# Performance work log

Measured on AMD Instinct MI355X. Metric: run time of the kernel, lower is better.

The kernel has to match this reference:

```python
import jax, jax.numpy as jnp
import numpy as np

EPS = 1e-5
KH = KW = 3  # deformable kernel
K = KH * KW


def _offset_conv(w, woff, boff):
    # standard 3x3 conv, stride 1, padding 1, NCHW
    out = jax.lax.conv_general_dilated(
        w, woff, window_strides=(1, 1), padding='SAME',
        dimension_numbers=('NCHW', 'OIHW', 'NCHW'))
    return out + boff[None, :, None, None]


def _deform_conv(feat, offset, wd, bd):
    # feat: [B,C,H,W]; offset: [B,2K,H,W] with (dy,dx) pairs per kernel point
    B, C, H, W = feat.shape
    off = offset.reshape(B, K, 2, H, W)
    ii = jnp.arange(H, dtype=feat.dtype)[:, None]  # [H,1]
    jj = jnp.arange(W, dtype=feat.dtype)[None, :]  # [1,W]
    kk = jnp.arange(K)
    ky = (kk // KW - 1).astype(feat.dtype)[None, :, None, None]  # [1,K,1,1]
    kx = (kk % KW - 1).astype(feat.dtype)[None, :, None, None]
    py = ii[None, None] + ky + off[:, :, 0]  # [B,K,H,W] sample rows
    px = jj[None, None] + kx + off[:, :, 1]  # [B,K,H,W] sample cols

    featf = feat.reshape(B, C, H * W)
    y0 = jnp.floor(py)
    x0 = jnp.floor(px)
    sampled = jnp.zeros((B, C, K, H, W), dtype=feat.dtype)
    for dy in (0, 1):
        for dx in (0, 1):
            yc = y0 + dy
            xc = x0 + dx
            wgt = (1.0 - jnp.abs(py - yc)) * (1.0 - jnp.abs(px - xc))
            valid = (yc >= 0) & (yc <= H - 1) & (xc >= 0) & (xc <= W - 1)
            wgt = jnp.where(valid, wgt, 0.0)  # zero padding outside
            yi = jnp.clip(yc, 0, H - 1).astype(jnp.int32)
            xi = jnp.clip(xc, 0, W - 1).astype(jnp.int32)
            idx = (yi * W + xi).reshape(B, 1, K * H * W)
            vals = jnp.take_along_axis(featf, idx, axis=2).reshape(B, C, K, H, W)
            sampled = sampled + vals * wgt[:, None]
    # weighted 3x3 conv over sampled points
    out = jnp.einsum('bckhw,ock->bohw', sampled, wd.reshape(wd.shape[0], C, K))
    return out + bd[None, :, None, None]


def setup_inputs() -> dict:
    key = jax.random.key(0)
    ks = jax.random.split(key, 13)
    B, Cin, H, W = 8, 256, 96, 96
    Cm = 64
    s1 = 1.0 / np.sqrt(Cin)
    s3 = 1.0 / np.sqrt(Cm * 9)
    return {
        'x': jax.random.normal(ks[0], (B, Cin, H, W), jnp.float32),
        'w1': jax.random.normal(ks[1], (Cm, Cin), jnp.float32) * s1,
        'b1': jax.random.normal(ks[2], (Cm,), jnp.float32) * s1,
        'woff': jax.random.normal(ks[3], (18, Cm, 3, 3), jnp.float32) * s3,
        'boff': jax.random.normal(ks[4], (18,), jnp.float32) * s3,
        'wd': jax.random.normal(ks[5], (Cm, Cm, 3, 3), jnp.float32) * s3,
        'bd': jax.random.normal(ks[6], (Cm,), jnp.float32) * s3,
        'gamma': jnp.ones((Cm,), jnp.float32),
        'beta': jnp.zeros((Cm,), jnp.float32),
        'rmean': jnp.zeros((Cm,), jnp.float32),
        'rvar': jax.random.uniform(ks[7], (Cm,), jnp.float32, 0.5, 1.5),
        'w2': jax.random.normal(ks[8], (Cin, Cm), jnp.float32) / np.sqrt(Cm),
        'b2': jax.random.normal(ks[9], (Cin,), jnp.float32) / np.sqrt(Cm),
    }


def reference(x, w1, b1, woff, boff, wd, bd, gamma, beta, rmean, rvar, w2, b2):
    # pwconv1 (1x1)
    w = jnp.einsum('bchw,oc->bohw', x, w1) + b1[None, :, None, None]
    # deformable 3x3 conv with predicted offsets
    off = _offset_conv(w, woff, boff)
    w = _deform_conv(w, off, wd, bd)
    # BatchNorm (eval mode, running stats)
    inv = gamma / jnp.sqrt(rvar + EPS)
    w = w * inv[None, :, None, None] + (beta - rmean * inv)[None, :, None, None]
    # pwconv2 (1x1) + sigmoid gate
    w = jnp.einsum('bchw,oc->bohw', w, w2) + b2[None, :, None, None]
    return x * jax.nn.sigmoid(w)
```

## Files before the change

### kernel.cpp

```cpp
#include <hip/hip_runtime.h>
#include <math.h>

#define H 96
#define W 96
#define HW 9216
#define B 8
#define CIN 256
#define CM 64
#define NPOS (B*HW)
#define NBLK (NPOS/64)

__device__ __forceinline__ int xswiz(int n) { return (n & 7) * 144 + (n >> 3); }

typedef float  f32x4  __attribute__((ext_vector_type(4)));
typedef short  bf16x8 __attribute__((ext_vector_type(8)));

#define OFF_WDBO  0
#define OFF_BNS   9216
#define OFF_BNB   9280
#define OFF_WDB1  9344
#define OFF_WDB3  17536
#define OFF_WDB2  35968
#define OFF_FCL   44160
#define OFF_OFFS  4762752
#define OFF_VCL   6089856

__device__ __forceinline__ unsigned bfbits(float f) {
  union { float f; unsigned u; } c;
  c.f = f;
  return (c.u + 0x7FFFu + ((c.u >> 16) & 1u)) >> 16;
}
__device__ __forceinline__ short f2bf(float f) { return (short)bfbits(f); }
__device__ __forceinline__ unsigned pack2(float lo, float hi) {
  return bfbits(lo) | (bfbits(hi) << 16);
}

__global__ __launch_bounds__(256) void k0_prep(
    const float* __restrict__ w1, const float* __restrict__ woff,
    const float* __restrict__ wd, const float* __restrict__ w2,
    const float* __restrict__ gamma, const float* __restrict__ beta,
    const float* __restrict__ rmean, const float* __restrict__ rvar,
    float* __restrict__ ws) {
  int i = blockIdx.x * 256 + threadIdx.x;
  if (i < 18432) {
    int j = i;
    int j8 = j & 7, lane = (j >> 3) & 63, nt = (j >> 9) & 1, kc = j >> 10;
    int n = nt * 16 + (lane & 15);
    int c = (kc & 1) * 32 + ((lane >> 4) & 3) * 8 + j8;
    int ks = kc >> 1;
    ((short*)(ws + OFF_WDBO))[j] = (n < 18) ? f2bf(woff[(n * 64 + c) * 9 + ks]) : (short)0;
  } else if (i < 18496) {
    int o = i - 18432;
    float inv = gamma[o] / sqrtf(rvar[o] + 1e-5f);
    ws[OFF_BNS + o] = inv;
    ws[OFF_BNB + o] = beta[o] - rmean[o] * inv;
  } else if (i < 34880) {
    int j = i - 18496;
    int j8 = j & 7, lane = (j >> 3) & 63, nt = (j >> 9) & 3, kc = j >> 11;
    int n = nt * 16 + (lane & 15);
    int c = kc * 32 + ((lane >> 4) & 3) * 8 + j8;
    ((short*)(ws + OFF_WDB1))[j] = f2bf(w1[n * 256 + c]);
  } else if (i < 71744) {
    int j = i - 34880;
    int j8 = j & 7, lane = (j >> 3) & 63, nt = (j >> 9) & 3, kc = j >> 11;
    int n = nt * 16 + (lane & 15);
    int c = (kc & 1) * 32 + ((lane >> 4) & 3) * 8 + j8;
    int ks = kc >> 1;
    ((short*)(ws + OFF_WDB3))[j] = f2bf(wd[(n * 64 + c) * 9 + ks]);
  } else if (i < 88128) {
    int j = i - 71744;
    int j8 = j & 7, lane = (j >> 3) & 63, nt = (j >> 9) & 15, kc = j >> 13;
    int n = nt * 16 + (lane & 15);
    int c = kc * 32 + ((lane >> 4) & 3) * 8 + j8;
    ((short*)(ws + OFF_WDB2))[j] = f2bf(w2[n * 64 + c]);
  }
}

__global__ __launch_bounds__(256) void k1_pw1(
    const float* __restrict__ x, const short* __restrict__ wdb1,
    const float* __restrict__ b1, float* __restrict__ fcl) {
  __shared__ float sA[64 * 66];
  int t = threadIdx.x;
  int lane = t & 63;
  int qq = __builtin_amdgcn_readfirstlane(t >> 6);
  int quad = lane >> 4, l15 = lane & 15;
  int gpos0 = xswiz(blockIdx.x) * 64;
  int b = gpos0 / HW, hw0 = gpos0 - b * HW;
  const float* xp = x + (size_t)b * CIN * HW + (size_t)(quad * 8) * HW + hw0 + qq * 16 + l15;

  float v[8][8];
#pragma unroll
  for (int kc = 0; kc < 8; kc++)
#pragma unroll
    for (int jj = 0; jj < 8; jj++)
      v[kc][jj] = xp[(size_t)(kc * 32 + jj) * HW];

  f32x4 acc[4];
#pragma unroll
  for (int nt = 0; nt < 4; nt++) acc[nt] = (f32x4){0.f, 0.f, 0.f, 0.f};
#pragma unroll
  for (int kc = 0; kc < 8; kc++) {
    union { unsigned u[4]; bf16x8 f; } af;
    af.u[0] = pack2(v[kc][0], v[kc][1]); af.u[1] = pack2(v[kc][2], v[kc][3]);
    af.u[2] = pack2(v[kc][4], v[kc][5]); af.u[3] = pack2(v[kc][6], v[kc][7]);
#pragma unroll
    for (int nt = 0; nt < 4; nt++) {
      bf16x8 bf = ((const bf16x8*)wdb1)[(kc * 4 + nt) * 64 + lane];
      acc[nt] = __builtin_amdgcn_mfma_f32_16x16x32_bf16(af.f, bf, acc[nt], 0, 0, 0);
    }
  }
#pragma unroll
  for (int nt = 0; nt < 4; nt++) {
    int o = nt * 16 + l15;
#pragma unroll
    for (int reg = 0; reg < 4; reg++) {
      int m = qq * 16 + quad * 4 + reg;
      sA[m * 66 + o] = acc[nt][reg] + b1[o];
    }
  }
  __syncthreads();
  for (int rr = t; rr < 4096; rr += 256) {
    int p2 = rr >> 6, o2 = rr & 63;
    fcl[(size_t)(gpos0 + p2) * 64 + o2] = sA[p2 * 66 + o2];
  }
}

__global__ __launch_bounds__(256) void k2_off(
    const float* __restrict__ fcl, const short* __restrict__ wdbo,
    const float* __restrict__ boff, float* __restrict__ offs) {
  __shared__ float sP[64 * 34];
  int t = threadIdx.x;
  int lane = t & 63;
  int qq = __builtin_amdgcn_readfirstlane(t >> 6);
  int quad = lane >> 4, l15 = lane & 15;
  int gpos0 = xswiz(blockIdx.x) * 64;
  int b = gpos0 / HW, hw0 = gpos0 - b * HW;
  int m = qq * 16 + l15;
  int hw = hw0 + m, i = hw / W, j = hw - i * W;
  const float* base = fcl + (size_t)(gpos0 + m) * 64 + quad * 8;

  f32x4 acc[2];
  acc[0] = (f32x4){0.f, 0.f, 0.f, 0.f};
  acc[1] = (f32x4){0.f, 0.f, 0.f, 0.f};

  f32x4 va0, vb0, va1, vb1;
  bool okc;
  {
    okc = (i >= 1) && (j >= 1);
    const float* s = base + (okc ? (-W - 1) * 64 : 0);
    va0 = *(const f32x4*)(s);      vb0 = *(const f32x4*)(s + 4);
    va1 = *(const f32x4*)(s + 32); vb1 = *(const f32x4*)(s + 36);
  }
#pragma unroll
  for (int ks = 0; ks < 9; ks++) {
    f32x4 z = (f32x4){0.f, 0.f, 0.f, 0.f};
    f32x4 a0 = okc ? va0 : z, c0 = okc ? vb0 : z;
    f32x4 a1 = okc ? va1 : z, c1 = okc ? vb1 : z;
    union { unsigned u[4]; bf16x8 f; } f0, f1;
    f0.u[0] = pack2(a0[0], a0[1]); f0.u[1] = pack2(a0[2], a0[3]);
    f0.u[2] = pack2(c0[0], c0[1]); f0.u[3] = pack2(c0[2], c0[3]);
    f1.u[0] = pack2(a1[0], a1[1]); f1.u[1] = pack2(a1[2], a1[3]);
    f1.u[2] = pack2(c1[0], c1[1]); f1.u[3] = pack2(c1[2], c1[3]);
    if (ks < 8) {
      int kn = ks + 1, dy = kn / 3 - 1, dx = kn % 3 - 1;
      okc = ((unsigned)(i + dy) < (unsigned)H) && ((unsigned)(j + dx) < (unsigned)W);
      const float* s = base + (okc ? (dy * W + dx) * 64 : 0);
      va0 = *(const f32x4*)(s);      vb0 = *(const f32x4*)(s + 4);
      va1 = *(const f32x4*)(s + 32); vb1 = *(const f32x4*)(s + 36);
    }
    bf16x8 bf00 = ((const bf16x8*)wdbo)[((ks * 2 + 0) * 2 + 0) * 64 + lane];
    bf16x8 bf01 = ((const bf16x8*)wdbo)[((ks * 2 + 0) * 2 + 1) * 64 + lane];
    bf16x8 bf10 = ((const bf16x8*)wdbo)[((ks * 2 + 1) * 2 + 0) * 64 + lane];
    bf16x8 bf11 = ((const bf16x8*)wdbo)[((ks * 2 + 1) * 2 + 1) * 64 + lane];
    acc[0] = __builtin_amdgcn_mfma_f32_16x16x32_bf16(f0.f, bf00, acc[0], 0, 0, 0);
    acc[1] = __builtin_amdgcn_mfma_f32_16x16x32_bf16(f0.f, bf01, acc[1], 0, 0, 0);
    acc[0] = __builtin_amdgcn_mfma_f32_16x16x32_bf16(f1.f, bf10, acc[0], 0, 0, 0);
    acc[1] = __builtin_amdgcn_mfma_f32_16x16x32_bf16(f1.f, bf11, acc[1], 0, 0, 0);
  }
#pragma unroll
  for (int nt = 0; nt < 2; nt++)
#pragma unroll
    for (int reg = 0; reg < 4; reg++) {
      int mm = qq * 16 + quad * 4 + reg;
      sP[mm * 34 + nt * 16 + l15] = acc[nt][reg];
    }
  __syncthreads();
  for (int rr = t; rr < 18 * 64; rr += 256) {
    int o = rr >> 6, p = rr & 63;
    offs[((size_t)b * 18 + o) * HW + hw0 + p] = sP[p * 34 + o] + boff[o];
  }
}

__global__ __launch_bounds__(256, 3) void k3_deform(
    const float* __restrict__ fcl, const float* __restrict__ offs,
    const short* __restrict__ wdb3, const float* __restrict__ bd,
    const float* __restrict__ bns, const float* __restrict__ bnb,
    short* __restrict__ vclb) {
  __shared__ __align__(16) short sAb[2][64 * 72];
  __shared__ __align__(16) int2 tiw[576][4];
  int t = threadIdx.x;
  int lane = t & 63;
  int qq = __builtin_amdgcn_readfirstlane(t >> 6);
  int quad = lane >> 4, l15 = lane & 15;
  int mrow = qq * 16 + l15;
  int gpos0 = xswiz(blockIdx.x) * 64;
  int b = gpos0 / HW, hw0 = gpos0 - b * HW;
  int hw = hw0 + lane;
  int i = hw / W, j = hw - i * W;
  const float* ob = offs + (size_t)b * 18 * HW + hw;

  for (int k = qq; k < 9; k += 4) {
    float dy = ob[(2 * k + 0) * HW];
    float dx = ob[(2 * k + 1) * HW];
    float py = (float)(i + k / 3 - 1) + dy;
    float px = (float)(j + k % 3 - 1) + dx;
    float y0f = floorf(py), x0f = floorf(px);
    int y0 = (int)y0f, x0 = (int)x0f;
    float fy = py - y0f, fx = px - x0f;
    float w00 = (1.f - fy) * (1.f - fx), w01 = (1.f - fy) * fx;
    float w10 = fy * (1.f - fx), w11 = fy * fx;
    bool vy0 = (y0 >= 0) && (y0 < H), vy1 = (y0 + 1 >= 0) && (y0 + 1 < H);
    bool vx0 = (x0 >= 0) && (x0 < W), vx1 = (x0 + 1 >= 0) && (x0 + 1 < W);
    if (!(vy0 && vx0)) w00 = 0.f;
    if (!(vy0 && vx1)) w01 = 0.f;
    if (!(vy1 && vx0)) w10 = 0.f;
    if (!(vy1 && vx1)) w11 = 0.f;
    int yi0 = min(max(y0, 0), H - 1), yi1 = min(max(y0 + 1, 0), H - 1);
    int xi0 = min(max(x0, 0), W - 1), xi1 = min(max(x0 + 1, 0), W - 1);
    int e = k * 64 + lane;
    tiw[e][0] = make_int2((yi0 * W + xi0) * 256, __float_as_int(w00));
    tiw[e][1] = make_int2((yi0 * W + xi1) * 256, __float_as_int(w01));
    tiw[e][2] = make_int2((yi1 * W + xi0) * 256, __float_as_int(w10));
    tiw[e][3] = make_int2((yi1 * W + xi1) * 256, __float_as_int(w11));
  }
  __syncthreads();

  const char* fb = (const char*)fcl + (size_t)b * HW * 256;
  int c2 = lane & 31;
  int c28 = c2 * 8;
  int half = lane >> 5;
  int parow = qq * 16 + half;

  float2 sv[8][4];
  float  sw[8][4];
  f32x4 acc[4];
#pragma unroll
  for (int nt = 0; nt < 4; nt++) acc[nt] = (f32x4){0.f, 0.f, 0.f, 0.f};

  auto issue = [&](int ks, int pp) {
    int e = ks * 64 + parow + pp * 2;
    int4 q0 = *(const int4*)&tiw[e][0];
    int4 q1 = *(const int4*)&tiw[e][2];
    sv[pp][0] = *(const float2*)(fb + (q0.x + c28)); sw[pp][0] = __int_as_float(q0.y);
    sv[pp][1] = *(const float2*)(fb + (q0.z + c28)); sw[pp][1] = __int_as_float(q0.w);
    sv[pp][2] = *(const float2*)(fb + (q1.x + c28)); sw[pp][2] = __int_as_float(q1.y);
    sv[pp][3] = *(const float2*)(fb + (q1.z + c28)); sw[pp][3] = __int_as_float(q1.w);
  };
  auto consume = [&](int pp, int bi) {
    int pa = parow + pp * 2;
    float slo = sw[pp][0] * sv[pp][0].x + sw[pp][1] * sv[pp][1].x +
                sw[pp][2] * sv[pp][2].x + sw[pp][3] * sv[pp][3].x;
    float shi = sw[pp][0] * sv[pp][0].y + sw[pp][1] * sv[pp][1].y +
                sw[pp][2] * sv[pp][2].y + sw[pp][3] * sv[pp][3].y;
    ((unsigned*)sAb[bi])[pa * 36 + c2] = pack2(slo, shi);
  };
  auto mfmastep = [&](int ks, int bi) {
#pragma unroll
    for (int ch = 0; ch < 2; ch++) {
      bf16x8 af = *(const bf16x8*)&sAb[bi][mrow * 72 + ch * 32 + quad * 8];
      int kc = ks * 2 + ch;
#pragma unroll
      for (int nt = 0; nt < 4; nt++) {
        bf16x8 bf = ((const bf16x8*)wdb3)[(kc * 4 + nt) * 64 + lane];
        acc[nt] = __builtin_amdgcn_mfma_f32_16x16x32_bf16(af, bf, acc[nt], 0, 0, 0);
      }
    }
  };

#pragma unroll
  for (int pp = 0; pp < 8; pp++) issue(0, pp);
  for (int ks = 0; ks < 8; ks++) {
    int bi = ks & 1;
#pragma unroll
    for (int pp = 0; pp < 8; pp++) {
      consume(pp, bi);
      issue(ks + 1, pp);
    }
    mfmastep(ks, bi);
  }
#pragma unroll
  for (int pp = 0; pp < 8; pp++) consume(pp, 0);
  mfmastep(8, 0);

  __syncthreads();
#pragma unroll
  for (int nt = 0; nt < 4; nt++) {
    int o = nt * 16 + l15;
    float sc = bns[o], sb = bnb[o], bb = bd[o];
#pragma unroll
    for (int reg = 0; reg < 4; reg++) {
      int m = qq * 16 + quad * 4 + reg;
      sAb[0][m * 72 + o] = f2bf((acc[nt][reg] + bb) * sc + sb);
    }
  }
  __syncthreads();
  for (int rr = t; rr < 2048; rr += 256) {
    int p = rr >> 5, cc = rr & 31;
    ((unsigned*)vclb)[(size_t)(gpos0 + p) * 32 + cc] = ((const unsigned*)sAb[0])[p * 36 + cc];
  }
}

__global__ __launch_bounds__(256) void k4_pw2(
    const float* __restrict__ x, const short* __restrict__ vclb,
    const short* __restrict__ wdb2, const float* __restrict__ b2,
    float* __restrict__ out) {
  __shared__ float sA[64 * 66];
  int t = threadIdx.x;
  int lane = t & 63;
  int qq = __builtin_amdgcn_readfirstlane(t >> 6);
  int quad = lane >> 4, l15 = lane & 15;
  int mrow = qq * 16 + l15;
  int gpos0 = xswiz(blockIdx.x) * 64;
  int b = gpos0 / HW, hw0 = gpos0 - b * HW;

  const bf16x8* ap = (const bf16x8*)(vclb + (size_t)(gpos0 + mrow) * 64);
  bf16x8 af0 = ap[quad];
  bf16x8 af1 = ap[4 + quad];

  f32x4 acc[16];
#pragma unroll
  for (int nt = 0; nt < 16; nt++) acc[nt] = (f32x4){0.f, 0.f, 0.f, 0.f};
#pragma unroll
  for (int nt = 0; nt < 16; nt++) {
    bf16x8 bf0 = ((const bf16x8*)wdb2)[(0 * 16 + nt) * 64 + lane];
    bf16x8 bf1 = ((const bf16x8*)wdb2)[(1 * 16 + nt) * 64 + lane];
    acc[nt] = __builtin_amdgcn_mfma_f32_16x16x32_bf16(af0, bf0, acc[nt], 0, 0, 0);
    acc[nt] = __builtin_amdgcn_mfma_f32_16x16x32_bf16(af1, bf1, acc[nt], 0, 0, 0);
  }
  for (int nc = 0; nc < 4; nc++) {
    __syncthreads();
#pragma unroll
    for (int nt2 = 0; nt2 < 4; nt2++) {
      int nt = nc * 4 + nt2;
      int o1 = nt2 * 16 + l15;
#pragma unroll
      for (int reg = 0; reg < 4; reg++) {
        int m = qq * 16 + quad * 4 + reg;
        sA[m * 66 + o1] = acc[nt][reg] + b2[nc * 64 + nt2 * 16 + l15];
      }
    }
    __syncthreads();
    for (int rr = t; rr < 4096; rr += 256) {
      int o1 = rr >> 6, p = rr & 63;
      int o = nc * 64 + o1;
      float wv = sA[p * 66 + o1];
      float sg = 1.f / (1.f + __expf(-wv));
      size_t gi = ((size_t)b * CIN + o) * HW + hw0 + p;
      out[gi] = x[gi] * sg;
    }
  }
}

extern "C" void kernel_launch(void* const* d_in, const int* in_sizes, int n_in,
                              void* d_out, int out_size, void* d_ws, size_t ws_size,
                              hipStream_t stream) {
  const float* x     = (const float*)d_in[0];
  const float* w1    = (const float*)d_in[1];
  const float* b1    = (const float*)d_in[2];
  const float* woff  = (const float*)d_in[3];
  const float* boff  = (const float*)d_in[4];
  const float* wd    = (const float*)d_in[5];
  const float* bd    = (const float*)d_in[6];
  const float* gamma = (const float*)d_in[7];
  const float* beta  = (const float*)d_in[8];
  const float* rmean = (const float*)d_in[9];
  const float* rvar  = (const float*)d_in[10];
  const float* w2    = (const float*)d_in[11];
  const float* b2    = (const float*)d_in[12];
  float* out = (float*)d_out;
  float* ws  = (float*)d_ws;

  dim3 blk(256);
  k0_prep<<<dim3(345), blk, 0, stream>>>(w1, woff, wd, w2, gamma, beta, rmean, rvar, ws);
  k1_pw1<<<dim3(NBLK), blk, 0, stream>>>(x, (const short*)(ws + OFF_WDB1), b1, ws + OFF_FCL);
  k2_off<<<dim3(NBLK), blk, 0, stream>>>(ws + OFF_FCL, (const short*)(ws + OFF_WDBO),
                                         boff, ws + OFF_OFFS);
  k3_deform<<<dim3(NBLK), blk, 0, stream>>>(ws + OFF_FCL, ws + OFF_OFFS,
                                            (const short*)(ws + OFF_WDB3), bd,
                                            ws + OFF_BNS, ws + OFF_BNB,
                                            (short*)(ws + OFF_VCL));
  k4_pw2<<<dim3(NBLK), blk, 0, stream>>>(x, (const short*)(ws + OFF_VCL),
                                         (const short*)(ws + OFF_WDB2), b2, out);
}
```

Before: 292.0 us.

## Fuse offset conv, deformable conv and pwconv2 into one kernel

Merges the offset-prediction, deformable-sampling and pointwise-conv2/sigmoid kernels into a single kernel working on the same 64-position tile. Offsets stay in shared memory and the BN-scaled deformable output stays in shared memory as bf16, instead of round-tripping through global workspace. Two shared regions are reused across the three stages, and a redundant barrier is dropped because each wave only touches its own rows. This cuts two launches and several MB of global traffic, but it raises register pressure from the 16-tile pw2 accumulator under a 3-block launch bound.

After: 334.1 us. +14.4%, slower.

```diff
diff --git a/kernel.cpp b/kernel.cpp
--- a/kernel.cpp
+++ b/kernel.cpp
@@ -22,8 +22,6 @@
 #define OFF_WDB3  17536
 #define OFF_WDB2  35968
 #define OFF_FCL   44160
-#define OFF_OFFS  4762752
-#define OFF_VCL   6089856
 
 __device__ __forceinline__ unsigned bfbits(float f) {
   union { float f; unsigned u; } c;
@@ -125,79 +123,15 @@
   }
 }
 
-__global__ __launch_bounds__(256) void k2_off(
+__global__ __launch_bounds__(256, 3) void k234(
     const float* __restrict__ fcl, const short* __restrict__ wdbo,
-    const float* __restrict__ boff, float* __restrict__ offs) {
-  __shared__ float sP[64 * 34];
-  int t = threadIdx.x;
-  int lane = t & 63;
-  int qq = __builtin_amdgcn_readfirstlane(t >> 6);
-  int quad = lane >> 4, l15 = lane & 15;
-  int gpos0 = xswiz(blockIdx.x) * 64;
-  int b = gpos0 / HW, hw0 = gpos0 - b * HW;
-  int m = qq * 16 + l15;
-  int hw = hw0 + m, i = hw / W, j = hw - i * W;
-  const float* base = fcl + (size_t)(gpos0 + m) * 64 + quad * 8;
-
-  f32x4 acc[2];
-  acc[0] = (f32x4){0.f, 0.f, 0.f, 0.f};
-  acc[1] = (f32x4){0.f, 0.f, 0.f, 0.f};
-
-  f32x4 va0, vb0, va1, vb1;
-  bool okc;
-  {
-    okc = (i >= 1) && (j >= 1);
-    const float* s = base + (okc ? (-W - 1) * 64 : 0);
-    va0 = *(const f32x4*)(s);      vb0 = *(const f32x4*)(s + 4);
-    va1 = *(const f32x4*)(s + 32); vb1 = *(const f32x4*)(s + 36);
-  }
-#pragma unroll
-  for (int ks = 0; ks < 9; ks++) {
-    f32x4 z = (f32x4){0.f, 0.f, 0.f, 0.f};
-    f32x4 a0 = okc ? va0 : z, c0 = okc ? vb0 : z;
-    f32x4 a1 = okc ? va1 : z, c1 = okc ? vb1 : z;
-    union { unsigned u[4]; bf16x8 f; } f0, f1;
-    f0.u[0] = pack2(a0[0], a0[1]); f0.u[1] = pack2(a0[2], a0[3]);
-    f0.u[2] = pack2(c0[0], c0[1]); f0.u[3] = pack2(c0[2], c0[3]);
-    f1.u[0] = pack2(a1[0], a1[1]); f1.u[1] = pack2(a1[2], a1[3]);
-    f1.u[2] = pack2(c1[0], c1[1]); f1.u[3] = pack2(c1[2], c1[3]);
-    if (ks < 8) {
-      int kn = ks + 1, dy = kn / 3 - 1, dx = kn % 3 - 1;
-      okc = ((unsigned)(i + dy) < (unsigned)H) && ((unsigned)(j + dx) < (unsigned)W);
-      const float* s = base + (okc ? (dy * W + dx) * 64 : 0);
-      va0 = *(const f32x4*)(s);      vb0 = *(const f32x4*)(s + 4);
-      va1 = *(const f32x4*)(s + 32); vb1 = *(const f32x4*)(s + 36);
-    }
-    bf16x8 bf00 = ((const bf16x8*)wdbo)[((ks * 2 + 0) * 2 + 0) * 64 + lane];
-    bf16x8 bf01 = ((const bf16x8*)wdbo)[((ks * 2 + 0) * 2 + 1) * 64 + lane];
-    bf16x8 bf10 = ((const bf16x8*)wdbo)[((ks * 2 + 1) * 2 + 0) * 64 + lane];
-    bf16x8 bf11 = ((const bf16x8*)wdbo)[((ks * 2 + 1) * 2 + 1) * 64 + lane];
-    acc[0] = __builtin_amdgcn_mfma_f32_16x16x32_bf16(f0.f, bf00, acc[0], 0, 0, 0);
-    acc[1] = __builtin_amdgcn_mfma_f32_16x16x32_bf16(f0.f, bf01, acc[1], 0, 0, 0);
-    acc[0] = __builtin_amdgcn_mfma_f32_16x16x32_bf16(f1.f, bf10, acc[0], 0, 0, 0);
-    acc[1] = __builtin_amdgcn_mfma_f32_16x16x32_bf16(f1.f, bf11, acc[1], 0, 0, 0);
-  }
-#pragma unroll
-  for (int nt = 0; nt < 2; nt++)
-#pragma unroll
-    for (int reg = 0; reg < 4; reg++) {
-      int mm = qq * 16 + quad * 4 + reg;
-      sP[mm * 34 + nt * 16 + l15] = acc[nt][reg];
-    }
-  __syncthreads();
-  for (int rr = t; rr < 18 * 64; rr += 256) {
-    int o = rr >> 6, p = rr & 63;
-    offs[((size_t)b * 18 + o) * HW + hw0 + p] = sP[p * 34 + o] + boff[o];
-  }
-}
-
-__global__ __launch_bounds__(256, 3) void k3_deform(
-    const float* __restrict__ fcl, const float* __restrict__ offs,
-    const short* __restrict__ wdb3, const float* __restrict__ bd,
-    const float* __restrict__ bns, const float* __restrict__ bnb,
-    short* __restrict__ vclb) {
-  __shared__ __align__(16) short sAb[2][64 * 72];
-  __shared__ __align__(16) int2 tiw[576][4];
+    const float* __restrict__ boff, const short* __restrict__ wdb3,
+    const float* __restrict__ bd, const float* __restrict__ bns,
+    const float* __restrict__ bnb, const short* __restrict__ wdb2,
+    const float* __restrict__ b2, const float* __restrict__ x,
+    float* __restrict__ out) {
+  __shared__ __align__(16) char R1[18432];
+  __shared__ __align__(16) char R2[18432];
   int t = threadIdx.x;
   int lane = t & 63;
   int qq = __builtin_amdgcn_readfirstlane(t >> 6);
@@ -205,36 +139,95 @@
   int mrow = qq * 16 + l15;
   int gpos0 = xswiz(blockIdx.x) * 64;
   int b = gpos0 / HW, hw0 = gpos0 - b * HW;
-  int hw = hw0 + lane;
-  int i = hw / W, j = hw - i * W;
-  const float* ob = offs + (size_t)b * 18 * HW + hw;
-
-  for (int k = qq; k < 9; k += 4) {
-    float dy = ob[(2 * k + 0) * HW];
-    float dx = ob[(2 * k + 1) * HW];
-    float py = (float)(i + k / 3 - 1) + dy;
-    float px = (float)(j + k % 3 - 1) + dx;
-    float y0f = floorf(py), x0f = floorf(px);
-    int y0 = (int)y0f, x0 = (int)x0f;
-    float fy = py - y0f, fx = px - x0f;
-    float w00 = (1.f - fy) * (1.f - fx), w01 = (1.f - fy) * fx;
-    float w10 = fy * (1.f - fx), w11 = fy * fx;
-    bool vy0 = (y0 >= 0) && (y0 < H), vy1 = (y0 + 1 >= 0) && (y0 + 1 < H);
-    bool vx0 = (x0 >= 0) && (x0 < W), vx1 = (x0 + 1 >= 0) && (x0 + 1 < W);
-    if (!(vy0 && vx0)) w00 = 0.f;
-    if (!(vy0 && vx1)) w01 = 0.f;
-    if (!(vy1 && vx0)) w10 = 0.f;
-    if (!(vy1 && vx1)) w11 = 0.f;
-    int yi0 = min(max(y0, 0), H - 1), yi1 = min(max(y0 + 1, 0), H - 1);
-    int xi0 = min(max(x0, 0), W - 1), xi1 = min(max(x0 + 1, 0), W - 1);
-    int e = k * 64 + lane;
-    tiw[e][0] = make_int2((yi0 * W + xi0) * 256, __float_as_int(w00));
-    tiw[e][1] = make_int2((yi0 * W + xi1) * 256, __float_as_int(w01));
-    tiw[e][2] = make_int2((yi1 * W + xi0) * 256, __float_as_int(w10));
-    tiw[e][3] = make_int2((yi1 * W + xi1) * 256, __float_as_int(w11));
+
+  {
+    int m = mrow;
+    int hw = hw0 + m, i = hw / W, j = hw - i * W;
+    const float* base = fcl + (size_t)(gpos0 + m) * 64 + quad * 8;
+    f32x4 acc2[2];
+    acc2[0] = (f32x4){0.f, 0.f, 0.f, 0.f};
+    acc2[1] = (f32x4){0.f, 0.f, 0.f, 0.f};
+
+    f32x4 va0, vb0, va1, vb1;
+    bool okc;
+    {
+      okc = (i >= 1) && (j >= 1);
+      const float* s = base + (okc ? (-W - 1) * 64 : 0);
+      va0 = *(const f32x4*)(s);      vb0 = *(const f32x4*)(s + 4);
+      va1 = *(const f32x4*)(s + 32); vb1 = *(const f32x4*)(s + 36);
+    }
+#pragma unroll
+    for (int ks = 0; ks < 9; ks++) {
+      f32x4 z = (f32x4){0.f, 0.f, 0.f, 0.f};
+      f32x4 a0 = okc ? va0 : z, c0 = okc ? vb0 : z;
+      f32x4 a1 = okc ? va1 : z, c1 = okc ? vb1 : z;
+      union { unsigned u[4]; bf16x8 f; } f0, f1;
+      f0.u[0] = pack2(a0[0], a0[1]); f0.u[1] = pack2(a0[2], a0[3]);
+      f0.u[2] = pack2(c0[0], c0[1]); f0.u[3] = pack2(c0[2], c0[3]);
+      f1.u[0] = pack2(a1[0], a1[1]); f1.u[1] = pack2(a1[2], a1[3]);
+      f1.u[2] = pack2(c1[0], c1[1]); f1.u[3] = pack2(c1[2], c1[3]);
+      if (ks < 8) {
+        int kn = ks + 1, dy = kn / 3 - 1, dx = kn % 3 - 1;
+        okc = ((unsigned)(i + dy) < (unsigned)H) && ((unsigned)(j + dx) < (unsigned)W);
+        const float* s = base + (okc ? (dy * W + dx) * 64 : 0);
+        va0 = *(const f32x4*)(s);      vb0 = *(const f32x4*)(s + 4);
+        va1 = *(const f32x4*)(s + 32); vb1 = *(const f32x4*)(s + 36);
+      }
+      bf16x8 bf00 = ((const bf16x8*)wdbo)[((ks * 2 + 0) * 2 + 0) * 64 + lane];
+      bf16x8 bf01 = ((const bf16x8*)wdbo)[((ks * 2 + 0) * 2 + 1) * 64 + lane];
+      bf16x8 bf10 = ((const bf16x8*)wdbo)[((ks * 2 + 1) * 2 + 0) * 64 + lane];
+      bf16x8 bf11 = ((const bf16x8*)wdbo)[((ks * 2 + 1) * 2 + 1) * 64 + lane];
+      acc2[0] = __builtin_amdgcn_mfma_f32_16x16x32_bf16(f0.f, bf00, acc2[0], 0, 0, 0);
+      acc2[1] = __builtin_amdgcn_mfma_f32_16x16x32_bf16(f0.f, bf01, acc2[1], 0, 0, 0);
+      acc2[0] = __builtin_amdgcn_mfma_f32_16x16x32_bf16(f1.f, bf10, acc2[0], 0, 0, 0);
+      acc2[1] = __builtin_amdgcn_mfma_f32_16x16x32_bf16(f1.f, bf11, acc2[1], 0, 0, 0);
+    }
+    float* sP = (float*)R2;
+    float bo0 = boff[l15];
+    float bo1 = (16 + l15 < 18) ? boff[16 + l15] : 0.f;
+#pragma unroll
+    for (int reg = 0; reg < 4; reg++) {
+      int mm = qq * 16 + quad * 4 + reg;
+      sP[mm * 34 + l15]      = acc2[0][reg] + bo0;
+      sP[mm * 34 + 16 + l15] = acc2[1][reg] + bo1;
+    }
   }
   __syncthreads();
 
+  {
+    const float* sP = (const float*)R2;
+    int2 (*tiw)[4] = (int2(*)[4])R1;
+    int hw = hw0 + lane;
+    int i = hw / W, j = hw - i * W;
+    for (int k = qq; k < 9; k += 4) {
+      float dy = sP[lane * 34 + 2 * k + 0];
+      float dx = sP[lane * 34 + 2 * k + 1];
+      float py = (float)(i + k / 3 - 1) + dy;
+      float px = (float)(j + k % 3 - 1) + dx;
+      float y0f = floorf(py), x0f = floorf(px);
+      int y0 = (int)y0f, x0 = (int)x0f;
+      float fy = py - y0f, fx = px - x0f;
+      float w00 = (1.f - fy) * (1.f - fx), w01 = (1.f - fy) * fx;
+      float w10 = fy * (1.f - fx), w11 = fy * fx;
+      bool vy0 = (y0 >= 0) && (y0 < H), vy1 = (y0 + 1 >= 0) && (y0 + 1 < H);
+      bool vx0 = (x0 >= 0) && (x0 < W), vx1 = (x0 + 1 >= 0) && (x0 + 1 < W);
+      if (!(vy0 && vx0)) w00 = 0.f;
+      if (!(vy0 && vx1)) w01 = 0.f;
+      if (!(vy1 && vx0)) w10 = 0.f;
+      if (!(vy1 && vx1)) w11 = 0.f;
+      int yi0 = min(max(y0, 0), H - 1), yi1 = min(max(y0 + 1, 0), H - 1);
+      int xi0 = min(max(x0, 0), W - 1), xi1 = min(max(x0 + 1, 0), W - 1);
+      int e = k * 64 + lane;
+      tiw[e][0] = make_int2((yi0 * W + xi0) * 256, __float_as_int(w00));
+      tiw[e][1] = make_int2((yi0 * W + xi1) * 256, __float_as_int(w01));
+      tiw[e][2] = make_int2((yi1 * W + xi0) * 256, __float_as_int(w10));
+      tiw[e][3] = make_int2((yi1 * W + xi1) * 256, __float_as_int(w11));
+    }
+  }
+  __syncthreads();
+
+  short* sAb = (short*)R2;
+  const int2 (*tiw)[4] = (const int2(*)[4])R1;
   const char* fb = (const char*)fcl + (size_t)b * HW * 256;
   int c2 = lane & 31;
   int c28 = c2 * 8;
@@ -243,9 +236,9 @@
 
   float2 sv[8][4];
   float  sw[8][4];
-  f32x4 acc[4];
-#pragma unroll
-  for (int nt = 0; nt < 4; nt++) acc[nt] = (f32x4){0.f, 0.f, 0.f, 0.f};
+  f32x4 acc3[4];
+#pragma unroll
+  for (int nt = 0; nt < 4; nt++) acc3[nt] = (f32x4){0.f, 0.f, 0.f, 0.f};
 
   auto issue = [&](int ks, int pp) {
     int e = ks * 64 + parow + pp * 2;
@@ -262,17 +255,17 @@
                 sw[pp][2] * sv[pp][2].x + sw[pp][3] * sv[pp][3].x;
     float shi = sw[pp][0] * sv[pp][0].y + sw[pp][1] * sv[pp][1].y +
                 sw[pp][2] * sv[pp][2].y + sw[pp][3] * sv[pp][3].y;
-    ((unsigned*)sAb[bi])[pa * 36 + c2] = pack2(slo, shi);
+    ((unsigned*)(sAb + bi * 64 * 72))[pa * 36 + c2] = pack2(slo, shi);
   };
   auto mfmastep = [&](int ks, int bi) {
 #pragma unroll
     for (int ch = 0; ch < 2; ch++) {
-      bf16x8 af = *(const bf16x8*)&sAb[bi][mrow * 72 + ch * 32 + quad * 8];
+      bf16x8 af = *(const bf16x8*)&sAb[bi * 64 * 72 + mrow * 72 + ch * 32 + quad * 8];
       int kc = ks * 2 + ch;
 #pragma unroll
       for (int nt = 0; nt < 4; nt++) {
         bf16x8 bf = ((const bf16x8*)wdb3)[(kc * 4 + nt) * 64 + lane];
-        acc[nt] = __builtin_amdgcn_mfma_f32_16x16x32_bf16(af, bf, acc[nt], 0, 0, 0);
+        acc3[nt] = __builtin_amdgcn_mfma_f32_16x16x32_bf16(af, bf, acc3[nt], 0, 0, 0);
       }
     }
   };
@@ -292,7 +285,6 @@
   for (int pp = 0; pp < 8; pp++) consume(pp, 0);
   mfmastep(8, 0);
 
-  __syncthreads();
 #pragma unroll
   for (int nt = 0; nt < 4; nt++) {
     int o = nt * 16 + l15;
@@ -300,43 +292,24 @@
 #pragma unroll
     for (int reg = 0; reg < 4; reg++) {
       int m = qq * 16 + quad * 4 + reg;
-      sAb[0][m * 72 + o] = f2bf((acc[nt][reg] + bb) * sc + sb);
-    }
-  }
-  __syncthreads();
-  for (int rr = t; rr < 2048; rr += 256) {
-    int p = rr >> 5, cc = rr & 31;
-    ((unsigned*)vclb)[(size_t)(gpos0 + p) * 32 + cc] = ((const unsigned*)sAb[0])[p * 36 + cc];
-  }
-}
-
-__global__ __launch_bounds__(256) void k4_pw2(
-    const float* __restrict__ x, const short* __restrict__ vclb,
-    const short* __restrict__ wdb2, const float* __restrict__ b2,
-    float* __restrict__ out) {
-  __shared__ float sA[64 * 66];
-  int t = threadIdx.x;
-  int lane = t & 63;
-  int qq = __builtin_amdgcn_readfirstlane(t >> 6);
-  int quad = lane >> 4, l15 = lane & 15;
-  int mrow = qq * 16 + l15;
-  int gpos0 = xswiz(blockIdx.x) * 64;
-  int b = gpos0 / HW, hw0 = gpos0 - b * HW;
-
-  const bf16x8* ap = (const bf16x8*)(vclb + (size_t)(gpos0 + mrow) * 64);
-  bf16x8 af0 = ap[quad];
-  bf16x8 af1 = ap[4 + quad];
-
-  f32x4 acc[16];
-#pragma unroll
-  for (int nt = 0; nt < 16; nt++) acc[nt] = (f32x4){0.f, 0.f, 0.f, 0.f};
+      sAb[m * 72 + o] = f2bf((acc3[nt][reg] + bb) * sc + sb);
+    }
+  }
+
+  bf16x8 af0 = *(const bf16x8*)&sAb[mrow * 72 + quad * 8];
+  bf16x8 af1 = *(const bf16x8*)&sAb[mrow * 72 + 32 + quad * 8];
+  f32x4 acc4[16];
+#pragma unroll
+  for (int nt = 0; nt < 16; nt++) acc4[nt] = (f32x4){0.f, 0.f, 0.f, 0.f};
 #pragma unroll
   for (int nt = 0; nt < 16; nt++) {
     bf16x8 bf0 = ((const bf16x8*)wdb2)[(0 * 16 + nt) * 64 + lane];
     bf16x8 bf1 = ((const bf16x8*)wdb2)[(1 * 16 + nt) * 64 + lane];
-    acc[nt] = __builtin_amdgcn_mfma_f32_16x16x32_bf16(af0, bf0, acc[nt], 0, 0, 0);
-    acc[nt] = __builtin_amdgcn_mfma_f32_16x16x32_bf16(af1, bf1, acc[nt], 0, 0, 0);
-  }
+    acc4[nt] = __builtin_amdgcn_mfma_f32_16x16x32_bf16(af0, bf0, acc4[nt], 0, 0, 0);
+    acc4[nt] = __builtin_amdgcn_mfma_f32_16x16x32_bf16(af1, bf1, acc4[nt], 0, 0, 0);
+  }
+
+  float* sA = (float*)R1;
   for (int nc = 0; nc < 4; nc++) {
     __syncthreads();
 #pragma unroll
@@ -346,7 +319,7 @@
 #pragma unroll
       for (int reg = 0; reg < 4; reg++) {
         int m = qq * 16 + quad * 4 + reg;
-        sA[m * 66 + o1] = acc[nt][reg] + b2[nc * 64 + nt2 * 16 + l15];
+        sA[m * 66 + o1] = acc4[nt][reg] + b2[nc * 64 + nt2 * 16 + l15];
       }
     }
     __syncthreads();
@@ -383,12 +356,8 @@
   dim3 blk(256);
   k0_prep<<<dim3(345), blk, 0, stream>>>(w1, woff, wd, w2, gamma, beta, rmean, rvar, ws);
   k1_pw1<<<dim3(NBLK), blk, 0, stream>>>(x, (const short*)(ws + OFF_WDB1), b1, ws + OFF_FCL);
-  k2_off<<<dim3(NBLK), blk, 0, stream>>>(ws + OFF_FCL, (const short*)(ws + OFF_WDBO),
-                                         boff, ws + OFF_OFFS);
-  k3_deform<<<dim3(NBLK), blk, 0, stream>>>(ws + OFF_FCL, ws + OFF_OFFS,
-                                            (const short*)(ws + OFF_WDB3), bd,
-                                            ws + OFF_BNS, ws + OFF_BNB,
-                                            (short*)(ws + OFF_VCL));
-  k4_pw2<<<dim3(NBLK), blk, 0, stream>>>(x, (const short*)(ws + OFF_VCL),
-                                         (const short*)(ws + OFF_WDB2), b2, out);
-}
+  k234<<<dim3(NBLK), blk, 0, stream>>>(ws + OFF_FCL, (const short*)(ws + OFF_WDBO), boff,
+                                       (const short*)(ws + OFF_WDB3), bd,
+                                       ws + OFF_BNS, ws + OFF_BNB,
+                                       (const short*)(ws + OFF_WDB2), b2, x, out);
+}
```
